# Performance work log

Hardware: AMD Instinct MI355X
Metric: run time of the kernel (lower is better)

## Reference

```python
import jax, jax.numpy as jnp
import numpy as np

N_NODES = 100000
N_GRAPHS = 64


def gcn_conv(x, edge_index, W, b, num_nodes):
    """PyG-style GCNConv: out = D^-1/2 (A + I) D^-1/2 (x @ W) + b."""
    # add self-loops
    loops = jnp.arange(num_nodes, dtype=edge_index.dtype)
    src = jnp.concatenate([edge_index[0], loops])  # [E+N]
    dst = jnp.concatenate([edge_index[1], loops])  # [E+N]
    # symmetric degree normalization (degree of target incl. self-loop)
    deg = jax.ops.segment_sum(jnp.ones_like(dst, dtype=x.dtype), dst,
                              num_segments=num_nodes)
    dinv = jax.lax.rsqrt(jnp.maximum(deg, 1.0))
    norm = dinv[src] * dinv[dst]  # [E+N]
    h = x @ W  # [N, out_dim] -- transform before propagation (fewer flops if out<in)
    msg = h[src] * norm[:, None]  # gather + scale
    out = jax.ops.segment_sum(msg, dst, num_segments=num_nodes)  # scatter-add
    return out + b


def global_mean_pool(x, batch, num_graphs):
    s = jax.ops.segment_sum(x, batch, num_segments=num_graphs)
    cnt = jax.ops.segment_sum(jnp.ones_like(batch, dtype=x.dtype), batch,
                              num_segments=num_graphs)
    return s / jnp.maximum(cnt, 1.0)[:, None]


def setup_inputs() -> dict:
    key = jax.random.key(0)
    k1, k2, k3, k4, k5, k6 = jax.random.split(key, 6)
    in_dim, hid_dim, out_dim = 128, 128, 64
    x = jax.random.normal(k1, (N_NODES, in_dim), dtype=jnp.float32)
    edge_index = jax.random.randint(k2, (2, 600000), 0, N_NODES, dtype=jnp.int64)
    batch = jnp.sort(jax.random.randint(k3, (N_NODES,), 0, N_GRAPHS, dtype=jnp.int64))
    W1 = jax.random.normal(k4, (in_dim, hid_dim), dtype=jnp.float32) / np.sqrt(in_dim)
    b1 = jnp.zeros((hid_dim,), dtype=jnp.float32)
    W2 = jax.random.normal(k5, (hid_dim, out_dim), dtype=jnp.float32) / np.sqrt(hid_dim)
    b2 = jnp.zeros((out_dim,), dtype=jnp.float32)
    return {"x": x, "edge_index": edge_index, "batch": batch,
            "W1": W1, "b1": b1, "W2": W2, "b2": b2}


def reference(x, edge_index, batch, W1, b1, W2, b2):
    h = jax.nn.relu(gcn_conv(x, edge_index, W1, b1, N_NODES))
    h = gcn_conv(h, edge_index, W2, b2, N_NODES)
    pooled = global_mean_pool(h, batch, N_GRAPHS)  # [n_graphs, out_dim]
    return jax.nn.sigmoid(pooled)
```

## Files before the change

kernel.cpp:

```cpp
#include <hip/hip_runtime.h>
#include <hip/hip_bf16.h>
#include <math.h>

static constexpr int NG   = 64;
static constexpr int DIN  = 128;
static constexpr int DHID = 128;
static constexpr int DOUT = 64;
static constexpr int CAP  = 32;

typedef short bf16x8 __attribute__((ext_vector_type(8)));
typedef float f32x4  __attribute__((ext_vector_type(4)));

__device__ __forceinline__ float bf2f(unsigned short u) {
  unsigned int x = ((unsigned int)u) << 16;
  return __builtin_bit_cast(float, x);
}
__device__ __forceinline__ unsigned short f2bf(float f) {
  unsigned int x = __builtin_bit_cast(unsigned int, f);
  unsigned int r = x + 0x7fffu + ((x >> 16) & 1u);
  return (unsigned short)(r >> 16);
}
__device__ __forceinline__ bf16x8 pack8(float4 a, float4 b) {
  bf16x8 r;
  r[0] = (short)f2bf(a.x); r[1] = (short)f2bf(a.y);
  r[2] = (short)f2bf(a.z); r[3] = (short)f2bf(a.w);
  r[4] = (short)f2bf(b.x); r[5] = (short)f2bf(b.y);
  r[6] = (short)f2bf(b.z); r[7] = (short)f2bf(b.w);
  return r;
}

__global__ void k_prep(int* __restrict__ cnt2, float* __restrict__ pool,
                       const float* __restrict__ W1, unsigned short* __restrict__ Wt1,
                       const float* __restrict__ W2, unsigned short* __restrict__ Wt2,
                       const int* __restrict__ batch, float* __restrict__ cnt, int N) {
  int i = blockIdx.x * blockDim.x + threadIdx.x;
  if (i < N) { cnt2[i] = 0; return; }
  i -= N;
  if (i < NG * DOUT) { pool[i] = 0.f; return; }
  i -= NG * DOUT;
  if (i < DHID * DIN) {
    int n = i / DIN, k = i % DIN;
    Wt1[i] = f2bf(W1[(size_t)k * DHID + n]);
    return;
  }
  i -= DHID * DIN;
  if (i < DOUT * DHID) {
    int n = i / DHID, k = i % DHID;
    Wt2[i] = f2bf(W2[(size_t)k * DOUT + n]);
    return;
  }
  i -= DOUT * DHID;
  if (i < NG) {
    int g = i;
    auto lower_bound = [&](int key) {
      int lo = 0, hi = N;
      while (lo < hi) {
        int mid = (lo + hi) >> 1;
        if (batch[mid] < key) lo = mid + 1; else hi = mid;
      }
      return lo;
    };
    cnt[g] = (float)(lower_bound(g + 1) - lower_bound(g));
  }
}

__global__ void k_fillc(const int* __restrict__ src, const int* __restrict__ dst,
                        int* __restrict__ cnt2, int* __restrict__ col, int E) {
  int i = blockIdx.x * blockDim.x + threadIdx.x;
  if (i < E) {
    int d = dst[i];
    int pos = atomicAdd(&cnt2[d], 1);
    if (pos < CAP) col[(size_t)d * CAP + pos] = src[i];
  }
}

__launch_bounds__(256)
__global__ void k_gemm1(const float* __restrict__ A, const unsigned short* __restrict__ Wt,
                        unsigned short* __restrict__ Cbf,
                        const int* __restrict__ cnt2, int M) {
  constexpr int K = 128, NC = 128, NT = NC / 16;
  __shared__ unsigned short Wlds[NC * K];
  const int tid = threadIdx.x;
  for (int c = tid; c < NC * K / 4; c += 256) {
    ushort4 v = *reinterpret_cast<const ushort4*>(Wt + c * 4);
    int n  = (c * 4) / K;
    int kb = ((c * 4) % K) * 2;
    *reinterpret_cast<ushort4*>((char*)Wlds + n * (K * 2) + (kb ^ ((n & 7) << 4))) = v;
  }
  __syncthreads();

  const int lane  = tid & 63;
  const int w     = tid >> 6;
  const int khalf = lane >> 4;
  const int r     = blockIdx.x * 64 + w * 16 + (lane & 15);
  const int rl    = min(r, M - 1);

  bf16x8 xf[K / 32];
  const float* Ar = A + (size_t)rl * K;
#pragma unroll
  for (int kk = 0; kk < K / 32; ++kk) {
    int kb = kk * 32 + khalf * 8;
    float4 v0 = *reinterpret_cast<const float4*>(Ar + kb);
    float4 v1 = *reinterpret_cast<const float4*>(Ar + kb + 4);
    xf[kk] = pack8(v0, v1);
  }

  f32x4 acc[NT] = {};
#pragma unroll
  for (int nt = 0; nt < NT; ++nt) {
    const int n = nt * 16 + (lane & 15);
    const char* wrow = (const char*)Wlds + n * (K * 2);
    const int sw = (n & 7) << 4;
#pragma unroll
    for (int kk = 0; kk < K / 32; ++kk) {
      int kb = (kk * 32 + khalf * 8) * 2;
      bf16x8 wf = *reinterpret_cast<const bf16x8*>(wrow + (kb ^ sw));
      acc[nt] = __builtin_amdgcn_mfma_f32_16x16x32_bf16(wf, xf[kk], acc[nt], 0, 0, 0);
    }
  }

  if (r < M) {
    float dv = rsqrtf((float)cnt2[r] + 1.0f);
    unsigned short* Crow = Cbf + (size_t)r * NC;
#pragma unroll
    for (int nt = 0; nt < NT; ++nt) {
      ushort4 o;
      o.x = f2bf(acc[nt][0] * dv); o.y = f2bf(acc[nt][1] * dv);
      o.z = f2bf(acc[nt][2] * dv); o.w = f2bf(acc[nt][3] * dv);
      *reinterpret_cast<ushort4*>(Crow + nt * 16 + khalf * 4) = o;
    }
  }
}

__launch_bounds__(256)
__global__ void k_gg2(const int* __restrict__ col, const int* __restrict__ cnt2,
                      const unsigned short* __restrict__ hbf1,
                      const unsigned short* __restrict__ Wt2,
                      const float* __restrict__ b1,
                      unsigned short* __restrict__ hbf2,
                      int N) {
  constexpr int K = 128, NC = 64, NT = NC / 16;
  __shared__ unsigned short Wlds[NC * K];
  __shared__ unsigned short Alds[64 * K];
  const int tid = threadIdx.x;
  for (int c = tid; c < NC * K / 4; c += 256) {
    ushort4 v = *reinterpret_cast<const ushort4*>(Wt2 + c * 4);
    int n  = (c * 4) / K;
    int kb = ((c * 4) % K) * 2;
    *reinterpret_cast<ushort4*>((char*)Wlds + n * (K * 2) + (kb ^ ((n & 7) << 4))) = v;
  }

  const int lane = tid & 63;
  const int w    = tid >> 6;
  const int sub  = lane >> 5;
  const int li   = lane & 31;
  const int base = blockIdx.x * 64;
  const size_t eoff = 4 * (size_t)li;

#pragma unroll
  for (int it = 0; it < 8; ++it) {
    int rloc = it * 8 + w * 2 + sub;
    int v = base + rloc;
    int vc = min(v, N - 1);
    ushort4 u = *reinterpret_cast<const ushort4*>(hbf1 + (size_t)vc * K + eoff);
    float a0 = bf2f(u.x), a1 = bf2f(u.y), a2 = bf2f(u.z), a3 = bf2f(u.w);
    int c = cnt2[vc];
    int deg = min(c, CAP);
    const int* cl = col + (size_t)vc * CAP;
    int j = 0;
    for (; j + 3 < deg; j += 4) {
      int s0 = cl[j], s1 = cl[j + 1], s2 = cl[j + 2], s3 = cl[j + 3];
      ushort4 u0 = *reinterpret_cast<const ushort4*>(hbf1 + (size_t)s0 * K + eoff);
      ushort4 u1 = *reinterpret_cast<const ushort4*>(hbf1 + (size_t)s1 * K + eoff);
      ushort4 u2 = *reinterpret_cast<const ushort4*>(hbf1 + (size_t)s2 * K + eoff);
      ushort4 u3 = *reinterpret_cast<const ushort4*>(hbf1 + (size_t)s3 * K + eoff);
      a0 += (bf2f(u0.x) + bf2f(u1.x)) + (bf2f(u2.x) + bf2f(u3.x));
      a1 += (bf2f(u0.y) + bf2f(u1.y)) + (bf2f(u2.y) + bf2f(u3.y));
      a2 += (bf2f(u0.z) + bf2f(u1.z)) + (bf2f(u2.z) + bf2f(u3.z));
      a3 += (bf2f(u0.w) + bf2f(u1.w)) + (bf2f(u2.w) + bf2f(u3.w));
    }
    for (; j < deg; ++j) {
      ushort4 uu = *reinterpret_cast<const ushort4*>(hbf1 + (size_t)cl[j] * K + eoff);
      a0 += bf2f(uu.x); a1 += bf2f(uu.y); a2 += bf2f(uu.z); a3 += bf2f(uu.w);
    }
    float dv = rsqrtf((float)c + 1.0f);
    float4 b = *reinterpret_cast<const float4*>(b1 + eoff);
    a0 = fmaxf(fmaf(a0, dv, b.x), 0.f);
    a1 = fmaxf(fmaf(a1, dv, b.y), 0.f);
    a2 = fmaxf(fmaf(a2, dv, b.z), 0.f);
    a3 = fmaxf(fmaf(a3, dv, b.w), 0.f);
    ushort4 o = make_ushort4(f2bf(a0), f2bf(a1), f2bf(a2), f2bf(a3));
    *reinterpret_cast<ushort4*>((char*)Alds + rloc * (K * 2) +
                                (int)((8 * li) ^ ((rloc & 7) << 4))) = o;
  }
  __syncthreads();

  const int khalf = lane >> 4;
  const int rloc  = w * 16 + (lane & 15);
  const int r     = base + rloc;
  bf16x8 xf[K / 32];
  const char* arow = (const char*)Alds + rloc * (K * 2);
  const int asw = (rloc & 7) << 4;
#pragma unroll
  for (int kk = 0; kk < K / 32; ++kk)
    xf[kk] = *reinterpret_cast<const bf16x8*>(arow + (((kk * 32 + khalf * 8) * 2) ^ asw));

  f32x4 acc[NT] = {};
#pragma unroll
  for (int nt = 0; nt < NT; ++nt) {
    const int n = nt * 16 + (lane & 15);
    const char* wrow = (const char*)Wlds + n * (K * 2);
    const int sw = (n & 7) << 4;
#pragma unroll
    for (int kk = 0; kk < K / 32; ++kk) {
      int kb = (kk * 32 + khalf * 8) * 2;
      bf16x8 wf = *reinterpret_cast<const bf16x8*>(wrow + (kb ^ sw));
      acc[nt] = __builtin_amdgcn_mfma_f32_16x16x32_bf16(wf, xf[kk], acc[nt], 0, 0, 0);
    }
  }

  if (r < N) {
    float dv = rsqrtf((float)cnt2[r] + 1.0f);
    unsigned short* Crow = hbf2 + (size_t)r * NC;
#pragma unroll
    for (int nt = 0; nt < NT; ++nt) {
      ushort4 o;
      o.x = f2bf(acc[nt][0] * dv); o.y = f2bf(acc[nt][1] * dv);
      o.z = f2bf(acc[nt][2] * dv); o.w = f2bf(acc[nt][3] * dv);
      *reinterpret_cast<ushort4*>(Crow + nt * 16 + khalf * 4) = o;
    }
  }
}

__global__ void k_gpool(const int* __restrict__ col, const int* __restrict__ cnt2,
                        const unsigned short* __restrict__ hbf2,
                        const int* __restrict__ batch,
                        float* __restrict__ pool, int N) {
  int wid  = (blockIdx.x * blockDim.x + threadIdx.x) >> 6;
  int lane = threadIdx.x & 63;
  int nw   = (gridDim.x * blockDim.x) >> 6;
  int per  = (N + nw - 1) / nw;
  int n0 = wid * per, n1 = min(n0 + per, N);
  if (n0 >= n1) return;
  int g = batch[n0];
  float pacc = 0.f;
  for (int v = n0; v < n1; ++v) {
    int bg = batch[v];
    if (bg != g) { atomicAdd(&pool[g * DOUT + lane], pacc); pacc = 0.f; g = bg; }
    float a = bf2f(hbf2[(size_t)v * DOUT + lane]);
    int c = cnt2[v];
    int deg = min(c, CAP);
    const int* cl = col + (size_t)v * CAP;
    int j = 0;
    for (; j + 3 < deg; j += 4) {
      int s0 = cl[j], s1 = cl[j + 1], s2 = cl[j + 2], s3 = cl[j + 3];
      float b0 = bf2f(hbf2[(size_t)s0 * DOUT + lane]);
      float b1v = bf2f(hbf2[(size_t)s1 * DOUT + lane]);
      float b2v = bf2f(hbf2[(size_t)s2 * DOUT + lane]);
      float b3 = bf2f(hbf2[(size_t)s3 * DOUT + lane]);
      a += (b0 + b1v) + (b2v + b3);
    }
    for (; j < deg; ++j) a += bf2f(hbf2[(size_t)cl[j] * DOUT + lane]);
    pacc += rsqrtf((float)c + 1.0f) * a;
  }
  atomicAdd(&pool[g * DOUT + lane], pacc);
}

__global__ void k_final(const float* __restrict__ pool, const float* __restrict__ cnt,
                        const float* __restrict__ b2, float* __restrict__ out) {
  int i = blockIdx.x * blockDim.x + threadIdx.x;
  if (i >= NG * DOUT) return;
  int g = i >> 6, c = i & 63;
  float cg = cnt[g];
  float v = (cg > 0.f) ? (pool[i] / cg + b2[c]) : 0.f;
  out[i] = 1.f / (1.f + expf(-v));
}

extern "C" void kernel_launch(void* const* d_in, const int* in_sizes, int n_in,
                              void* d_out, int out_size, void* d_ws, size_t ws_size,
                              hipStream_t stream) {
  const float* x    = (const float*)d_in[0];
  const int*   ei   = (const int*)d_in[1];
  const int*   bat  = (const int*)d_in[2];
  const float* W1   = (const float*)d_in[3];
  const float* b1   = (const float*)d_in[4];
  const float* W2   = (const float*)d_in[5];
  const float* b2   = (const float*)d_in[6];
  float* out = (float*)d_out;

  const int N = in_sizes[0] / DIN;
  const int E = in_sizes[1] / 2;
  const int* src = ei;
  const int* dst = ei + E;

  char* wp = (char*)d_ws;
  auto alloc = [&](size_t bytes) { char* r = wp; wp += (bytes + 15) & ~(size_t)15; return r; };
  int*   cnt2 = (int*)  alloc(sizeof(int) * N);
  int*   col  = (int*)  alloc(sizeof(int) * (size_t)N * CAP);
  float* cnt  = (float*)alloc(sizeof(float) * NG);
  float* pool = (float*)alloc(sizeof(float) * NG * DOUT);
  unsigned short* Wt1  = (unsigned short*)alloc(sizeof(unsigned short) * DHID * DIN);
  unsigned short* Wt2  = (unsigned short*)alloc(sizeof(unsigned short) * DOUT * DHID);
  unsigned short* hbf1 = (unsigned short*)alloc(sizeof(unsigned short) * (size_t)N * DHID);
  unsigned short* hbf2 = (unsigned short*)alloc(sizeof(unsigned short) * (size_t)N * DOUT);

  const int B256 = 256;
  auto cdiv = [](int a, int b) { return (a + b - 1) / b; };

  const int prepN = N + NG * DOUT + DHID * DIN + DOUT * DHID + NG;
  k_prep<<<cdiv(prepN, B256), B256, 0, stream>>>(cnt2, pool, W1, Wt1, W2, Wt2, bat, cnt, N);

  k_fillc<<<cdiv(E, B256), B256, 0, stream>>>(src, dst, cnt2, col, E);

  k_gemm1<<<cdiv(N, 64), B256, 0, stream>>>(x, Wt1, hbf1, cnt2, N);

  k_gg2<<<cdiv(N, 64), B256, 0, stream>>>(col, cnt2, hbf1, Wt2, b1, hbf2, N);

  k_gpool<<<1024, B256, 0, stream>>>(col, cnt2, hbf2, bat, pool, N);

  k_final<<<cdiv(NG * DOUT, B256), B256, 0, stream>>>(pool, cnt, b2, out);
}
```

Before: 277.3 us.

## Split fused gather-GEMM and gather-pool into separate gather, GEMM and pool kernels

Replaces the fused layer-2 gather+GEMM kernel and the fused gather+pool kernel with standalone gather kernels that load eight masked neighbours at a time, a templated MFMA GEMM that takes bf16 input, and a simple streaming pool kernel. The aim is more memory-level parallelism and occupancy in the gathers, since the fused kernels carried large LDS and a serial per-wave loop in pooling. The cost is extra launches and extra round trips of intermediate bf16 activations through global memory. Padded neighbour slots are clamped and masked, so reads go past deg but stay within CAP.

```diff
diff --git a/kernel.cpp b/kernel.cpp
--- a/kernel.cpp
+++ b/kernel.cpp
@@ -74,11 +74,13 @@
   }
 }
 
+template<int NC, bool ABF16>
 __launch_bounds__(256)
-__global__ void k_gemm1(const float* __restrict__ A, const unsigned short* __restrict__ Wt,
-                        unsigned short* __restrict__ Cbf,
-                        const int* __restrict__ cnt2, int M) {
-  constexpr int K = 128, NC = 128, NT = NC / 16;
+__global__ void k_gemm_mfma(const void* __restrict__ Av, const unsigned short* __restrict__ Wt,
+                            unsigned short* __restrict__ Cbf,
+                            const int* __restrict__ cnt2, int M) {
+  constexpr int K = 128;
+  constexpr int NT = NC / 16;
   __shared__ unsigned short Wlds[NC * K];
   const int tid = threadIdx.x;
   for (int c = tid; c < NC * K / 4; c += 256) {
@@ -96,13 +98,20 @@
   const int rl    = min(r, M - 1);
 
   bf16x8 xf[K / 32];
-  const float* Ar = A + (size_t)rl * K;
-#pragma unroll
-  for (int kk = 0; kk < K / 32; ++kk) {
-    int kb = kk * 32 + khalf * 8;
-    float4 v0 = *reinterpret_cast<const float4*>(Ar + kb);
-    float4 v1 = *reinterpret_cast<const float4*>(Ar + kb + 4);
-    xf[kk] = pack8(v0, v1);
+  if constexpr (ABF16) {
+    const unsigned short* Ar = (const unsigned short*)Av + (size_t)rl * K;
+#pragma unroll
+    for (int kk = 0; kk < K / 32; ++kk)
+      xf[kk] = *reinterpret_cast<const bf16x8*>(Ar + kk * 32 + khalf * 8);
+  } else {
+    const float* Ar = (const float*)Av + (size_t)rl * K;
+#pragma unroll
+    for (int kk = 0; kk < K / 32; ++kk) {
+      int kb = kk * 32 + khalf * 8;
+      float4 v0 = *reinterpret_cast<const float4*>(Ar + kb);
+      float4 v1 = *reinterpret_cast<const float4*>(Ar + kb + 4);
+      xf[kk] = pack8(v0, v1);
+    }
   }
 
   f32x4 acc[NT] = {};
@@ -132,109 +141,59 @@
   }
 }
 
-__launch_bounds__(256)
-__global__ void k_gg2(const int* __restrict__ col, const int* __restrict__ cnt2,
-                      const unsigned short* __restrict__ hbf1,
-                      const unsigned short* __restrict__ Wt2,
-                      const float* __restrict__ b1,
-                      unsigned short* __restrict__ hbf2,
-                      int N) {
-  constexpr int K = 128, NC = 64, NT = NC / 16;
-  __shared__ unsigned short Wlds[NC * K];
-  __shared__ unsigned short Alds[64 * K];
-  const int tid = threadIdx.x;
-  for (int c = tid; c < NC * K / 4; c += 256) {
-    ushort4 v = *reinterpret_cast<const ushort4*>(Wt2 + c * 4);
-    int n  = (c * 4) / K;
-    int kb = ((c * 4) % K) * 2;
-    *reinterpret_cast<ushort4*>((char*)Wlds + n * (K * 2) + (kb ^ ((n & 7) << 4))) = v;
-  }
-
-  const int lane = tid & 63;
-  const int w    = tid >> 6;
-  const int sub  = lane >> 5;
-  const int li   = lane & 31;
-  const int base = blockIdx.x * 64;
+template<int D, bool RELU_BIAS>
+__global__ void k_gather8(const int* __restrict__ col, const int* __restrict__ cnt2,
+                          const unsigned short* __restrict__ hbf,
+                          unsigned short* __restrict__ outbf,
+                          const float* __restrict__ bias, int N) {
+  constexpr int LPR = D / 4;
+  constexpr int NPW = 64 / LPR;
+  int wid  = (blockIdx.x * blockDim.x + threadIdx.x) >> 6;
+  int lane = threadIdx.x & 63;
+  int sub  = lane / LPR;
+  int li   = lane % LPR;
+  int v = wid * NPW + sub;
+  if (v >= N) return;
   const size_t eoff = 4 * (size_t)li;
-
-#pragma unroll
-  for (int it = 0; it < 8; ++it) {
-    int rloc = it * 8 + w * 2 + sub;
-    int v = base + rloc;
-    int vc = min(v, N - 1);
-    ushort4 u = *reinterpret_cast<const ushort4*>(hbf1 + (size_t)vc * K + eoff);
-    float a0 = bf2f(u.x), a1 = bf2f(u.y), a2 = bf2f(u.z), a3 = bf2f(u.w);
-    int c = cnt2[vc];
-    int deg = min(c, CAP);
-    const int* cl = col + (size_t)vc * CAP;
-    int j = 0;
-    for (; j + 3 < deg; j += 4) {
-      int s0 = cl[j], s1 = cl[j + 1], s2 = cl[j + 2], s3 = cl[j + 3];
-      ushort4 u0 = *reinterpret_cast<const ushort4*>(hbf1 + (size_t)s0 * K + eoff);
-      ushort4 u1 = *reinterpret_cast<const ushort4*>(hbf1 + (size_t)s1 * K + eoff);
-      ushort4 u2 = *reinterpret_cast<const ushort4*>(hbf1 + (size_t)s2 * K + eoff);
-      ushort4 u3 = *reinterpret_cast<const ushort4*>(hbf1 + (size_t)s3 * K + eoff);
-      a0 += (bf2f(u0.x) + bf2f(u1.x)) + (bf2f(u2.x) + bf2f(u3.x));
-      a1 += (bf2f(u0.y) + bf2f(u1.y)) + (bf2f(u2.y) + bf2f(u3.y));
-      a2 += (bf2f(u0.z) + bf2f(u1.z)) + (bf2f(u2.z) + bf2f(u3.z));
-      a3 += (bf2f(u0.w) + bf2f(u1.w)) + (bf2f(u2.w) + bf2f(u3.w));
-    }
-    for (; j < deg; ++j) {
-      ushort4 uu = *reinterpret_cast<const ushort4*>(hbf1 + (size_t)cl[j] * K + eoff);
-      a0 += bf2f(uu.x); a1 += bf2f(uu.y); a2 += bf2f(uu.z); a3 += bf2f(uu.w);
-    }
-    float dv = rsqrtf((float)c + 1.0f);
-    float4 b = *reinterpret_cast<const float4*>(b1 + eoff);
-    a0 = fmaxf(fmaf(a0, dv, b.x), 0.f);
-    a1 = fmaxf(fmaf(a1, dv, b.y), 0.f);
-    a2 = fmaxf(fmaf(a2, dv, b.z), 0.f);
-    a3 = fmaxf(fmaf(a3, dv, b.w), 0.f);
-    ushort4 o = make_ushort4(f2bf(a0), f2bf(a1), f2bf(a2), f2bf(a3));
-    *reinterpret_cast<ushort4*>((char*)Alds + rloc * (K * 2) +
-                                (int)((8 * li) ^ ((rloc & 7) << 4))) = o;
-  }
-  __syncthreads();
-
-  const int khalf = lane >> 4;
-  const int rloc  = w * 16 + (lane & 15);
-  const int r     = base + rloc;
-  bf16x8 xf[K / 32];
-  const char* arow = (const char*)Alds + rloc * (K * 2);
-  const int asw = (rloc & 7) << 4;
-#pragma unroll
-  for (int kk = 0; kk < K / 32; ++kk)
-    xf[kk] = *reinterpret_cast<const bf16x8*>(arow + (((kk * 32 + khalf * 8) * 2) ^ asw));
-
-  f32x4 acc[NT] = {};
-#pragma unroll
-  for (int nt = 0; nt < NT; ++nt) {
-    const int n = nt * 16 + (lane & 15);
-    const char* wrow = (const char*)Wlds + n * (K * 2);
-    const int sw = (n & 7) << 4;
-#pragma unroll
-    for (int kk = 0; kk < K / 32; ++kk) {
-      int kb = (kk * 32 + khalf * 8) * 2;
-      bf16x8 wf = *reinterpret_cast<const bf16x8*>(wrow + (kb ^ sw));
-      acc[nt] = __builtin_amdgcn_mfma_f32_16x16x32_bf16(wf, xf[kk], acc[nt], 0, 0, 0);
-    }
-  }
-
-  if (r < N) {
-    float dv = rsqrtf((float)cnt2[r] + 1.0f);
-    unsigned short* Crow = hbf2 + (size_t)r * NC;
-#pragma unroll
-    for (int nt = 0; nt < NT; ++nt) {
-      ushort4 o;
-      o.x = f2bf(acc[nt][0] * dv); o.y = f2bf(acc[nt][1] * dv);
-      o.z = f2bf(acc[nt][2] * dv); o.w = f2bf(acc[nt][3] * dv);
-      *reinterpret_cast<ushort4*>(Crow + nt * 16 + khalf * 4) = o;
-    }
-  }
-}
-
-__global__ void k_gpool(const int* __restrict__ col, const int* __restrict__ cnt2,
-                        const unsigned short* __restrict__ hbf2,
-                        const int* __restrict__ batch,
+  int c   = cnt2[v];
+  int deg = min(c, CAP);
+  const int* cl = col + (size_t)v * CAP;
+  ushort4 u = *reinterpret_cast<const ushort4*>(hbf + (size_t)v * D + eoff);
+  float a0 = bf2f(u.x), a1 = bf2f(u.y), a2 = bf2f(u.z), a3 = bf2f(u.w);
+  for (int j = 0; j < deg; j += 8) {
+    int4 i0 = *reinterpret_cast<const int4*>(cl + j);
+    int4 i1 = *reinterpret_cast<const int4*>(cl + j + 4);
+    int   s[8] = {i0.x, i0.y, i0.z, i0.w, i1.x, i1.y, i1.z, i1.w};
+    float m[8];
+#pragma unroll
+    for (int k = 0; k < 8; ++k) {
+      m[k] = (j + k < deg) ? 1.f : 0.f;
+      s[k] = min(max(s[k], 0), N - 1);
+    }
+    ushort4 r[8];
+#pragma unroll
+    for (int k = 0; k < 8; ++k)
+      r[k] = *reinterpret_cast<const ushort4*>(hbf + (size_t)s[k] * D + eoff);
+#pragma unroll
+    for (int k = 0; k < 8; ++k) {
+      a0 = fmaf(m[k], bf2f(r[k].x), a0);
+      a1 = fmaf(m[k], bf2f(r[k].y), a1);
+      a2 = fmaf(m[k], bf2f(r[k].z), a2);
+      a3 = fmaf(m[k], bf2f(r[k].w), a3);
+    }
+  }
+  float dv = rsqrtf((float)c + 1.0f);
+  a0 *= dv; a1 *= dv; a2 *= dv; a3 *= dv;
+  if (RELU_BIAS) {
+    float4 b = *reinterpret_cast<const float4*>(bias + eoff);
+    a0 = fmaxf(a0 + b.x, 0.f); a1 = fmaxf(a1 + b.y, 0.f);
+    a2 = fmaxf(a2 + b.z, 0.f); a3 = fmaxf(a3 + b.w, 0.f);
+  }
+  ushort4 o = make_ushort4(f2bf(a0), f2bf(a1), f2bf(a2), f2bf(a3));
+  *reinterpret_cast<ushort4*>(outbf + (size_t)v * D + eoff) = o;
+}
+
+__global__ void k_pool2(const unsigned short* __restrict__ out2, const int* __restrict__ batch,
                         float* __restrict__ pool, int N) {
   int wid  = (blockIdx.x * blockDim.x + threadIdx.x) >> 6;
   int lane = threadIdx.x & 63;
@@ -243,27 +202,24 @@
   int n0 = wid * per, n1 = min(n0 + per, N);
   if (n0 >= n1) return;
   int g = batch[n0];
-  float pacc = 0.f;
-  for (int v = n0; v < n1; ++v) {
-    int bg = batch[v];
-    if (bg != g) { atomicAdd(&pool[g * DOUT + lane], pacc); pacc = 0.f; g = bg; }
-    float a = bf2f(hbf2[(size_t)v * DOUT + lane]);
-    int c = cnt2[v];
-    int deg = min(c, CAP);
-    const int* cl = col + (size_t)v * CAP;
-    int j = 0;
-    for (; j + 3 < deg; j += 4) {
-      int s0 = cl[j], s1 = cl[j + 1], s2 = cl[j + 2], s3 = cl[j + 3];
-      float b0 = bf2f(hbf2[(size_t)s0 * DOUT + lane]);
-      float b1v = bf2f(hbf2[(size_t)s1 * DOUT + lane]);
-      float b2v = bf2f(hbf2[(size_t)s2 * DOUT + lane]);
-      float b3 = bf2f(hbf2[(size_t)s3 * DOUT + lane]);
-      a += (b0 + b1v) + (b2v + b3);
-    }
-    for (; j < deg; ++j) a += bf2f(hbf2[(size_t)cl[j] * DOUT + lane]);
-    pacc += rsqrtf((float)c + 1.0f) * a;
-  }
-  atomicAdd(&pool[g * DOUT + lane], pacc);
+  float acc = 0.f;
+  int n = n0;
+  while (n < n1) {
+    if (n + 4 <= n1 && batch[n + 3] == g) {
+      float a0 = bf2f(out2[(size_t)(n + 0) * DOUT + lane]);
+      float a1 = bf2f(out2[(size_t)(n + 1) * DOUT + lane]);
+      float a2 = bf2f(out2[(size_t)(n + 2) * DOUT + lane]);
+      float a3 = bf2f(out2[(size_t)(n + 3) * DOUT + lane]);
+      acc += (a0 + a1) + (a2 + a3);
+      n += 4;
+    } else {
+      int bg = batch[n];
+      if (bg != g) { atomicAdd(&pool[g * DOUT + lane], acc); acc = 0.f; g = bg; }
+      acc += bf2f(out2[(size_t)n * DOUT + lane]);
+      ++n;
+    }
+  }
+  atomicAdd(&pool[g * DOUT + lane], acc);
 }
 
 __global__ void k_final(const float* __restrict__ pool, const float* __restrict__ cnt,
@@ -299,10 +255,12 @@
   int*   col  = (int*)  alloc(sizeof(int) * (size_t)N * CAP);
   float* cnt  = (float*)alloc(sizeof(float) * NG);
   float* pool = (float*)alloc(sizeof(float) * NG * DOUT);
-  unsigned short* Wt1  = (unsigned short*)alloc(sizeof(unsigned short) * DHID * DIN);
-  unsigned short* Wt2  = (unsigned short*)alloc(sizeof(unsigned short) * DOUT * DHID);
-  unsigned short* hbf1 = (unsigned short*)alloc(sizeof(unsigned short) * (size_t)N * DHID);
-  unsigned short* hbf2 = (unsigned short*)alloc(sizeof(unsigned short) * (size_t)N * DOUT);
+  unsigned short* Wt1    = (unsigned short*)alloc(sizeof(unsigned short) * DHID * DIN);
+  unsigned short* Wt2    = (unsigned short*)alloc(sizeof(unsigned short) * DOUT * DHID);
+  unsigned short* hbf1   = (unsigned short*)alloc(sizeof(unsigned short) * (size_t)N * DHID);
+  unsigned short* out1bf = (unsigned short*)alloc(sizeof(unsigned short) * (size_t)N * DHID);
+  unsigned short* hbf2   = hbf1;
+  unsigned short* out2bf = out1bf;
 
   const int B256 = 256;
   auto cdiv = [](int a, int b) { return (a + b - 1) / b; };
@@ -312,11 +270,17 @@
 
   k_fillc<<<cdiv(E, B256), B256, 0, stream>>>(src, dst, cnt2, col, E);
 
-  k_gemm1<<<cdiv(N, 64), B256, 0, stream>>>(x, Wt1, hbf1, cnt2, N);
-
-  k_gg2<<<cdiv(N, 64), B256, 0, stream>>>(col, cnt2, hbf1, Wt2, b1, hbf2, N);
-
-  k_gpool<<<1024, B256, 0, stream>>>(col, cnt2, hbf2, bat, pool, N);
+  k_gemm_mfma<DHID, false><<<cdiv(N, 64), B256, 0, stream>>>(x, Wt1, hbf1, cnt2, N);
+
+  k_gather8<DHID, true><<<cdiv(cdiv(N, 2) * 64, B256), B256, 0, stream>>>(
+      col, cnt2, hbf1, out1bf, b1, N);
+
+  k_gemm_mfma<DOUT, true><<<cdiv(N, 64), B256, 0, stream>>>(out1bf, Wt2, hbf2, cnt2, N);
+
+  k_gather8<DOUT, false><<<cdiv(cdiv(N, 4) * 64, B256), B256, 0, stream>>>(
+      col, cnt2, hbf2, out2bf, nullptr, N);
+
+  k_pool2<<<1024, B256, 0, stream>>>(out2bf, bat, pool, N);
 
   k_final<<<cdiv(NG * DOUT, B256), B256, 0, stream>>>(pool, cnt, b2, out);
 }
```

After: 222.3 us. 1.25x faster.
